# Kernel tuning notes

Hardware: AMD Instinct MI355X
Metric: run time of the kernel (lower is better)

Reference implementation:

```python
import jax, jax.numpy as jnp
import numpy as np

N, E, IN_DIM, OUT_DIM, N_GRAPHS = 50000, 400000, 64, 128, 64


def setup_inputs() -> dict:
    key = jax.random.key(0)
    ks = jax.random.split(key, 16)
    x = jax.random.normal(ks[0], (N, IN_DIM), dtype=jnp.float32)
    edge_index = jax.random.randint(ks[1], (2, E), 0, N, dtype=jnp.int32)
    batch = jnp.sort(jax.random.randint(ks[2], (N,), 0, N_GRAPHS, dtype=jnp.int32))

    def glorot(k, shape):
        lim = np.sqrt(6.0 / (shape[0] + shape[1]))
        return jax.random.uniform(k, shape, jnp.float32, -lim, lim)

    d = IN_DIM
    return {
        "x": x, "edge_index": edge_index, "batch": batch,
        "W1": glorot(ks[3], (d, 2 * d)),     "b1": jnp.zeros((2 * d,), jnp.float32),
        "W2": glorot(ks[4], (2 * d, 4 * d)), "b2": jnp.zeros((4 * d,), jnp.float32),
        "W3": glorot(ks[5], (d, 2 * d)),     "b3": jnp.zeros((2 * d,), jnp.float32),
        "W4": glorot(ks[6], (2 * d, 4 * d)), "b4": jnp.zeros((4 * d,), jnp.float32),
        "W7": glorot(ks[7], (9 * d, OUT_DIM)), "b7": jnp.zeros((OUT_DIM,), jnp.float32),
    }


def _gcn_conv(x, W, b, src, dst, dis):
    # GCNConv: x' = D^{-1/2} (A + I) D^{-1/2} (x W) + b
    h = x @ W                                   # [N, F]
    norm = dis[src] * dis[dst]                  # [E]
    agg = jax.ops.segment_sum(h[src] * norm[:, None], dst, num_segments=N)
    agg = agg + h * (dis * dis)[:, None]        # self-loop contribution
    return agg + b


def reference(x, edge_index, batch, W1, b1, W2, b2, W3, b3, W4, b4, W7, b7):
    src, dst = edge_index[0], edge_index[1]
    # degree of A + I (PyG counts in-degree over columns, +1 for self-loop)
    deg = jax.ops.segment_sum(jnp.ones((E,), x.dtype), dst, num_segments=N) + 1.0
    dis = jax.lax.rsqrt(deg)

    i1 = jnp.tanh(_gcn_conv(x, W1, b1, src, dst, dis))
    i1 = jnp.tanh(_gcn_conv(i1, W2, b2, src, dst, dis))
    i1 = jax.ops.segment_max(i1, batch, num_segments=N_GRAPHS)  # global_max_pool
    i1 = jnp.max(i1, axis=0, keepdims=True)                     # [1, 4d]
    i1 = jnp.broadcast_to(i1, (x.shape[0], i1.shape[1]))        # expand to [N, 4d]

    i2 = jnp.tanh(_gcn_conv(x, W3, b3, src, dst, dis))
    i2 = jnp.tanh(_gcn_conv(i2, W4, b4, src, dst, dis))

    c = jnp.concatenate((i1, i2, x), axis=1)                    # [N, 9d]
    return jnp.tanh(_gcn_conv(c, W7, b7, src, dst, dis))
```

## Files before the change

kernel.cpp:

```cpp
#include <hip/hip_runtime.h>
#include <hip/hip_bf16.h>
#include <cstdint>
#include <cstddef>

#define NN 50000
#define EE 400000

typedef __attribute__((ext_vector_type(8))) __bf16 bf16x8;
typedef __attribute__((ext_vector_type(4))) __bf16 bf16x4;
typedef __attribute__((ext_vector_type(2))) __bf16 bf16x2;
typedef __attribute__((ext_vector_type(4))) float f32x4;

static __device__ __forceinline__ float dec_key(unsigned k) {
  return (k & 0x80000000u) ? __uint_as_float(k & 0x7fffffffu) : __uint_as_float(~k);
}
static __device__ __forceinline__ unsigned enc_key(float f) {
  unsigned b = __float_as_uint(f);
  return (f >= 0.f) ? (b | 0x80000000u) : ~b;
}

__global__ void count_kernel(const int* __restrict__ dst, int* __restrict__ cnt, int e) {
  int i = blockIdx.x * blockDim.x + threadIdx.x;
  if (i < e) atomicAdd(&cnt[dst[i]], 1);
}

__global__ void dis_kernel(const int* __restrict__ cnt, float* __restrict__ dis, int n) {
  int i = blockIdx.x * blockDim.x + threadIdx.x;
  if (i < n) dis[i] = rsqrtf((float)cnt[i] + 1.0f);
}

#define SCAN_CHUNK 1024
__global__ __launch_bounds__(256) void scan1_kernel(const int* __restrict__ cnt,
                                                    int* __restrict__ rowptr,
                                                    int* __restrict__ bsum, int n) {
  int b = blockIdx.x;
  int base = b * SCAN_CHUNK;
  int t = threadIdx.x;
  int v[4];
  int s = 0;
#pragma unroll
  for (int i = 0; i < 4; ++i) {
    int idx = base + t * 4 + i;
    v[i] = (idx < n) ? cnt[idx] : 0;
    s += v[i];
  }
  int lane = t & 63, w = t >> 6;
  int inc = s;
#pragma unroll
  for (int off = 1; off < 64; off <<= 1) {
    int o = __shfl_up(inc, off, 64);
    if (lane >= off) inc += o;
  }
  __shared__ int wsum[4];
  if (lane == 63) wsum[w] = inc;
  __syncthreads();
  int woff = 0;
  for (int i = 0; i < w; ++i) woff += wsum[i];
  int run = woff + inc - s;
#pragma unroll
  for (int i = 0; i < 4; ++i) {
    int idx = base + t * 4 + i;
    if (idx < n) rowptr[idx] = run;
    run += v[i];
  }
  if (t == 255) bsum[b] = woff + inc;
}

__global__ void scan2_kernel(int* __restrict__ bsum, int nb) {
  int t = threadIdx.x;
  int v = (t < nb) ? bsum[t] : 0;
  int s = v;
#pragma unroll
  for (int off = 1; off < 64; off <<= 1) {
    int o = __shfl_up(s, off, 64);
    if (t >= off) s += o;
  }
  if (t < nb) bsum[t] = s - v;
}

__global__ __launch_bounds__(256) void scan3_kernel(int* __restrict__ rowptr,
                                                    const int* __restrict__ bsum, int n, int total) {
  int i = blockIdx.x * blockDim.x + threadIdx.x;
  if (i < n) rowptr[i] += bsum[i >> 10];
  if (i == 0) rowptr[n] = total;
}

__global__ void fill_kernel(const int* __restrict__ src, const int* __restrict__ dst,
                            const int* __restrict__ rowptr, int* __restrict__ cursor,
                            int* __restrict__ col, int e) {
  int i = blockIdx.x * blockDim.x + threadIdx.x;
  if (i < e) {
    int d = dst[i];
    int p = atomicAdd(&cursor[d], 1);
    col[rowptr[d] + p] = src[i];
  }
}

__global__ __launch_bounds__(256) void wcvt_kernel(const float* __restrict__ W,
                                                   __bf16* __restrict__ Wt, int K, int Nout) {
  int idx = blockIdx.x * blockDim.x + threadIdx.x;
  if (idx < K * Nout) {
    int n = idx / K, k = idx - n * K;
    Wt[idx] = (__bf16)W[(size_t)k * Nout + n];
  }
}

__global__ __launch_bounds__(256) void wcat_kernel(const float* __restrict__ W1,
                                                   const float* __restrict__ W3,
                                                   const float* __restrict__ b1,
                                                   const float* __restrict__ b3,
                                                   float* __restrict__ Wcat,
                                                   float* __restrict__ bcat) {
  int idx = blockIdx.x * blockDim.x + threadIdx.x;
  if (idx < 64 * 256) {
    int k = idx >> 8, j = idx & 255;
    Wcat[idx] = (j < 128) ? W1[k * 128 + j] : W3[k * 128 + (j - 128)];
  }
  if (idx < 256) bcat[idx] = (idx < 128) ? b1[idx] : b3[idx - 128];
}

#define BM 64
#define BN 64
#define BK 16

template <typename OT>
__global__ __launch_bounds__(256) void gemm_f32(
    const float* __restrict__ A, const float* __restrict__ W, OT* __restrict__ C,
    int M, int K, int Nout, const float* __restrict__ colAdd, int accumulate, int doTanh) {
  __shared__ float As[BK][BM + 4];
  __shared__ float Ws[BK][BN];
  int tid = threadIdx.x;
  int row0 = blockIdx.x * BM;
  int col0 = blockIdx.y * BN;
  int tx = tid & 15;
  int ty = tid >> 4;
  float acc[4][4] = {};
  for (int k0 = 0; k0 < K; k0 += BK) {
#pragma unroll
    for (int i = 0; i < 4; ++i) {
      int idx = tid + i * 256;
      int r = idx >> 4, c = idx & 15;
      int gr = row0 + r;
      float v = (gr < M) ? A[(size_t)gr * K + k0 + c] : 0.f;
      As[c][r] = v;
    }
#pragma unroll
    for (int i = 0; i < 4; ++i) {
      int idx = tid + i * 256;
      int r = idx >> 6, c = idx & 63;
      Ws[r][c] = W[(size_t)(k0 + r) * Nout + col0 + c];
    }
    __syncthreads();
#pragma unroll
    for (int kk = 0; kk < BK; ++kk) {
      float4 av = *(const float4*)&As[kk][ty * 4];
      float4 wv = *(const float4*)&Ws[kk][tx * 4];
      float a[4] = {av.x, av.y, av.z, av.w};
      float w[4] = {wv.x, wv.y, wv.z, wv.w};
#pragma unroll
      for (int i = 0; i < 4; ++i)
#pragma unroll
        for (int j = 0; j < 4; ++j) acc[i][j] = fmaf(a[i], w[j], acc[i][j]);
    }
    __syncthreads();
  }
#pragma unroll
  for (int i = 0; i < 4; ++i) {
    int gr = row0 + ty * 4 + i;
    if (gr >= M) continue;
#pragma unroll
    for (int j = 0; j < 4; ++j) {
      int gc = col0 + tx * 4 + j;
      size_t idx = (size_t)gr * Nout + gc;
      float v = acc[i][j];
      if (colAdd) v += colAdd[gc];
      if (accumulate) v += (float)C[idx];
      if (doTanh) v = tanhf(v);
      C[idx] = (OT)v;
    }
  }
}

#define TM 128
#define TN 64
#define TK 64

__global__ __launch_bounds__(256) void gemm_mfma(
    const __bf16* __restrict__ A, int lda, const __bf16* __restrict__ Wt,
    float* __restrict__ Cf, __bf16* __restrict__ Ch,
    int M, int K, int Nout, const float* __restrict__ colAdd, int doTanh,
    unsigned* __restrict__ colmaxOut) {
  __shared__ char lds[(TM * TK + TN * TK) * 2];
  char* AsB = lds;
  char* BtB = lds + TM * TK * 2;
  int tid = threadIdx.x;
  int row0 = blockIdx.x * TM;
  int col0 = blockIdx.y * TN;
  int w = tid >> 6, l = tid & 63;
  int lr = l & 15, lh = l >> 4;
  int wmB = (w >> 1) * 64;
  int wnB = (w & 1) * 32;
  f32x4 acc[4][2] = {};
  for (int k0 = 0; k0 < K; k0 += TK) {
    if (k0) __syncthreads();
#pragma unroll
    for (int i = 0; i < 4; ++i) {
      int id = tid + i * 256;
      int r = id >> 3, oc = id & 7;
      int gr = row0 + r;
      bf16x8 sv;
      if (gr < M) sv = *(const bf16x8*)(A + (size_t)gr * lda + k0 + oc * 8);
      else sv = bf16x8{};
      int byte = (r * 128 + oc * 16) ^ ((r & 7) << 4);
      *(bf16x8*)(AsB + byte) = sv;
    }
#pragma unroll
    for (int i = 0; i < 2; ++i) {
      int id = tid + i * 256;
      int c = id >> 3, oc = id & 7;
      bf16x8 sv = *(const bf16x8*)(Wt + (size_t)(col0 + c) * K + k0 + oc * 8);
      int byte = (c * 128 + oc * 16) ^ ((c & 7) << 4);
      *(bf16x8*)(BtB + byte) = sv;
    }
    __syncthreads();
#pragma unroll
    for (int s = 0; s < 2; ++s) {
      bf16x8 af[4], bfr[2];
#pragma unroll
      for (int mi = 0; mi < 4; ++mi) {
        int r = wmB + mi * 16 + lr;
        int byte = (r * 128 + (s * 32 + lh * 8) * 2) ^ ((r & 7) << 4);
        af[mi] = *(const bf16x8*)(AsB + byte);
      }
#pragma unroll
      for (int ni = 0; ni < 2; ++ni) {
        int c = wnB + ni * 16 + lr;
        int byte = (c * 128 + (s * 32 + lh * 8) * 2) ^ ((c & 7) << 4);
        bfr[ni] = *(const bf16x8*)(BtB + byte);
      }
#pragma unroll
      for (int mi = 0; mi < 4; ++mi)
#pragma unroll
        for (int ni = 0; ni < 2; ++ni)
          acc[mi][ni] =
              __builtin_amdgcn_mfma_f32_16x16x32_bf16(af[mi], bfr[ni], acc[mi][ni], 0, 0, 0);
    }
  }
  float cmax[2] = {-3.0e38f, -3.0e38f};
#pragma unroll
  for (int mi = 0; mi < 4; ++mi) {
#pragma unroll
    for (int ni = 0; ni < 2; ++ni) {
#pragma unroll
      for (int r = 0; r < 4; ++r) {
        int gr = row0 + wmB + mi * 16 + lh * 4 + r;
        if (gr >= M) continue;
        int gc = col0 + wnB + ni * 16 + lr;
        size_t idx = (size_t)gr * Nout + gc;
        float v = acc[mi][ni][r];
        if (colAdd) v += colAdd[gc];
        if (doTanh) v = tanhf(v);
        if (colmaxOut) cmax[ni] = fmaxf(cmax[ni], v);
        if (Cf) Cf[idx] = v;
        if (Ch) Ch[idx] = (__bf16)v;
      }
    }
  }
  if (colmaxOut) {
#pragma unroll
    for (int ni = 0; ni < 2; ++ni) {
      float m = cmax[ni];
      m = fmaxf(m, __shfl_xor(m, 16));
      m = fmaxf(m, __shfl_xor(m, 32));
      if (lh == 0) {
        int gc = col0 + wnB + ni * 16 + lr;
        atomicMax(&colmaxOut[gc], enc_key(m));
      }
    }
  }
}

template <int VEC, typename IT>
static __device__ __forceinline__ void loadrow(const IT* p, float (&f)[VEC]) {
  if constexpr (sizeof(IT) == 4) {
    if constexpr (VEC == 4) {
      float4 h = *(const float4*)p;
      f[0] = h.x; f[1] = h.y; f[2] = h.z; f[3] = h.w;
    } else if constexpr (VEC == 2) {
      float2 h = *(const float2*)p;
      f[0] = h.x; f[1] = h.y;
    } else {
      f[0] = p[0];
    }
  } else {
    if constexpr (VEC == 4) {
      bf16x4 h = *(const bf16x4*)p;
      f[0] = (float)h[0]; f[1] = (float)h[1]; f[2] = (float)h[2]; f[3] = (float)h[3];
    } else if constexpr (VEC == 2) {
      bf16x2 h = *(const bf16x2*)p;
      f[0] = (float)h[0]; f[1] = (float)h[1];
    } else {
      f[0] = (float)p[0];
    }
  }
}

template <int F, bool EPI, typename IT, typename OT>
__global__ __launch_bounds__(256) void agg_kernel(
    const IT* __restrict__ H, const int* __restrict__ rowptr, const int* __restrict__ col,
    const float* __restrict__ dis, const float* __restrict__ bias, OT* __restrict__ out, int n) {
  constexpr int VEC = F / 64;
  int wid = (int)((blockIdx.x * blockDim.x + threadIdx.x) >> 6);
  int lane = threadIdx.x & 63;
  if (wid >= n) return;
  int node = __builtin_amdgcn_readfirstlane(wid);
  float dd = dis[node];
  float acc[VEC];
  {
    float h[VEC];
    loadrow<VEC, IT>(H + (size_t)node * F + lane * VEC, h);
#pragma unroll
    for (int i = 0; i < VEC; ++i) acc[i] = h[i] * dd * dd;
  }
  int beg = rowptr[node], end = rowptr[node + 1];
  for (int e = beg; e < end; ++e) {
    int s = col[e];
    float w = dis[s] * dd;
    float h[VEC];
    loadrow<VEC, IT>(H + (size_t)s * F + lane * VEC, h);
#pragma unroll
    for (int i = 0; i < VEC; ++i) acc[i] = fmaf(h[i], w, acc[i]);
  }
  OT* o = out + (size_t)node * F + lane * VEC;
#pragma unroll
  for (int i = 0; i < VEC; ++i) {
    float v = acc[i];
    if constexpr (EPI) v = tanhf(v + bias[lane * VEC + i]);
    o[i] = (OT)v;
  }
}

__global__ __launch_bounds__(128) void crow_kernel(const unsigned* __restrict__ maxkey,
                                                   const float* __restrict__ W7top,
                                                   float* __restrict__ crow) {
  int j = threadIdx.x;
  float s = 0.f;
  for (int f = 0; f < 256; ++f) s = fmaf(tanhf(dec_key(maxkey[f])), W7top[f * 128 + j], s);
  crow[j] = s;
}

extern "C" void kernel_launch(void* const* d_in, const int* in_sizes, int n_in,
                              void* d_out, int out_size, void* d_ws, size_t ws_size,
                              hipStream_t stream) {
  const float* x  = (const float*)d_in[0];
  const int* ei   = (const int*)d_in[1];
  const int* srcp = ei;
  const int* dstp = ei + EE;
  const float* W1 = (const float*)d_in[3];
  const float* b1 = (const float*)d_in[4];
  const float* W2 = (const float*)d_in[5];
  const float* b2 = (const float*)d_in[6];
  const float* W3 = (const float*)d_in[7];
  const float* b3 = (const float*)d_in[8];
  const float* W4 = (const float*)d_in[9];
  const float* b4 = (const float*)d_in[10];
  const float* W7 = (const float*)d_in[11];
  const float* b7 = (const float*)d_in[12];
  float* out = (float*)d_out;

  char* p = (char*)d_ws;
  auto alloc = [&](size_t bytes) -> void* {
    void* r = (void*)p;
    p += (bytes + 255) & ~(size_t)255;
    return r;
  };
  __bf16* T13  = (__bf16*)alloc((size_t)NN * 256 * 2);
  float*  H    = (float*)alloc((size_t)NN * 128 * 4);
  __bf16* Hb13 = (__bf16*)alloc((size_t)NN * 256 * 2);
  __bf16* Bb   = (__bf16*)alloc((size_t)NN * 256 * 2);
  float*  AX   = (float*)alloc((size_t)NN * 64 * 4);
  __bf16* W2t  = (__bf16*)alloc((size_t)256 * 128 * 2);
  __bf16* W4t  = (__bf16*)alloc((size_t)256 * 128 * 2);
  __bf16* W7t  = (__bf16*)alloc((size_t)128 * 256 * 2);
  float*  Wcat = (float*)alloc((size_t)64 * 256 * 4);
  float*  bcat = (float*)alloc(256 * 4);
  float* dis = (float*)alloc((size_t)NN * 4);
  int* cnt = (int*)alloc((size_t)NN * 4);
  int* cursor = (int*)alloc((size_t)NN * 4);
  int* rowptr = (int*)alloc((size_t)(NN + 1) * 4);
  int* col = (int*)alloc((size_t)EE * 4);
  int* bsum = (int*)alloc(64 * 4);
  unsigned* maxkey = (unsigned*)alloc(256 * 4);
  float* crow = (float*)alloc(128 * 4);

  hipMemsetAsync(cnt, 0, (size_t)NN * 4, stream);
  hipMemsetAsync(cursor, 0, (size_t)NN * 4, stream);
  hipMemsetAsync(maxkey, 0, 256 * 4, stream);

  int eb = (EE + 255) / 256;
  int nb = (NN + 255) / 256;
  int nchunks = (NN + SCAN_CHUNK - 1) / SCAN_CHUNK;
  count_kernel<<<eb, 256, 0, stream>>>(dstp, cnt, EE);
  dis_kernel<<<nb, 256, 0, stream>>>(cnt, dis, NN);
  scan1_kernel<<<nchunks, 256, 0, stream>>>(cnt, rowptr, bsum, NN);
  scan2_kernel<<<1, 64, 0, stream>>>(bsum, nchunks);
  scan3_kernel<<<nb, 256, 0, stream>>>(rowptr, bsum, NN, EE);
  fill_kernel<<<eb, 256, 0, stream>>>(srcp, dstp, rowptr, cursor, col, EE);

  wcvt_kernel<<<(256 * 128 + 255) / 256, 256, 0, stream>>>(W2, W2t, 128, 256);
  wcvt_kernel<<<(256 * 128 + 255) / 256, 256, 0, stream>>>(W4, W4t, 128, 256);
  wcvt_kernel<<<(128 * 256 + 255) / 256, 256, 0, stream>>>(W7 + 256 * 128, W7t, 256, 128);
  wcat_kernel<<<(64 * 256 + 255) / 256, 256, 0, stream>>>(W1, W3, b1, b3, Wcat, bcat);

  dim3 gB(256);
  int mrows = (NN + BM - 1) / BM;
  int mrowsT = (NN + TM - 1) / TM;
  int aggB = (NN + 3) / 4;

  agg_kernel<64, false, float, float><<<aggB, gB, 0, stream>>>(x, rowptr, col, dis, nullptr, AX, NN);
  gemm_f32<__bf16><<<dim3(mrows, 4), gB, 0, stream>>>(AX, Wcat, T13, NN, 64, 256, bcat, 0, 1);
  agg_kernel<256, false, __bf16, __bf16><<<aggB, gB, 0, stream>>>(T13, rowptr, col, dis, nullptr, Hb13, NN);
  gemm_mfma<<<dim3(mrowsT, 4), gB, 0, stream>>>(Hb13, 256, W2t, nullptr, nullptr, NN, 128, 256, b2, 0, maxkey);
  gemm_mfma<<<dim3(mrowsT, 4), gB, 0, stream>>>(Hb13 + 128, 256, W4t, nullptr, Bb, NN, 128, 256, b4, 1, nullptr);
  crow_kernel<<<1, 128, 0, stream>>>(maxkey, W7, crow);
  gemm_mfma<<<dim3(mrowsT, 2), gB, 0, stream>>>(Bb, 256, W7t, H, nullptr, NN, 256, 128, crow, 0, nullptr);
  gemm_f32<float><<<dim3(mrows, 2), gB, 0, stream>>>(x, W7 + 512 * 128, H, NN, 64, 128, nullptr, 1, 0);
  agg_kernel<128, true, float, float><<<aggB, gB, 0, stream>>>(H, rowptr, col, dis, b7, out, NN);
}
```

Baseline: 457.4 us.

## Replace atomic column max with per-block partials and halve MFMA row tile

The first MFMA GEMM no longer does a global atomicMax on encoded keys. Each block instead writes its per-wave column maxima to a partial buffer, and a new colreduce kernel reduces those partials, which removes the atomics and the memset. The MFMA row tile also shrinks from 128 to 64 rows, giving twice as many blocks with fewer accumulators each. In exchange this adds a kernel launch and a partial buffer, and weight-tile reuse per block drops.

```diff
diff --git a/kernel.cpp b/kernel.cpp
--- a/kernel.cpp
+++ b/kernel.cpp
@@ -10,14 +10,6 @@
 typedef __attribute__((ext_vector_type(4))) __bf16 bf16x4;
 typedef __attribute__((ext_vector_type(2))) __bf16 bf16x2;
 typedef __attribute__((ext_vector_type(4))) float f32x4;
-
-static __device__ __forceinline__ float dec_key(unsigned k) {
-  return (k & 0x80000000u) ? __uint_as_float(k & 0x7fffffffu) : __uint_as_float(~k);
-}
-static __device__ __forceinline__ unsigned enc_key(float f) {
-  unsigned b = __float_as_uint(f);
-  return (f >= 0.f) ? (b | 0x80000000u) : ~b;
-}
 
 __global__ void count_kernel(const int* __restrict__ dst, int* __restrict__ cnt, int e) {
   int i = blockIdx.x * blockDim.x + threadIdx.x;
@@ -181,15 +173,16 @@
   }
 }
 
-#define TM 128
+#define TM 64
 #define TN 64
 #define TK 64
+#define CSLOTS 1568
 
 __global__ __launch_bounds__(256) void gemm_mfma(
     const __bf16* __restrict__ A, int lda, const __bf16* __restrict__ Wt,
     float* __restrict__ Cf, __bf16* __restrict__ Ch,
     int M, int K, int Nout, const float* __restrict__ colAdd, int doTanh,
-    unsigned* __restrict__ colmaxOut) {
+    float* __restrict__ colmaxPart) {
   __shared__ char lds[(TM * TK + TN * TK) * 2];
   char* AsB = lds;
   char* BtB = lds + TM * TK * 2;
@@ -198,13 +191,13 @@
   int col0 = blockIdx.y * TN;
   int w = tid >> 6, l = tid & 63;
   int lr = l & 15, lh = l >> 4;
-  int wmB = (w >> 1) * 64;
+  int wmB = (w >> 1) * 32;
   int wnB = (w & 1) * 32;
-  f32x4 acc[4][2] = {};
+  f32x4 acc[2][2] = {};
   for (int k0 = 0; k0 < K; k0 += TK) {
     if (k0) __syncthreads();
 #pragma unroll
-    for (int i = 0; i < 4; ++i) {
+    for (int i = 0; i < 2; ++i) {
       int id = tid + i * 256;
       int r = id >> 3, oc = id & 7;
       int gr = row0 + r;
@@ -225,9 +218,9 @@
     __syncthreads();
 #pragma unroll
     for (int s = 0; s < 2; ++s) {
-      bf16x8 af[4], bfr[2];
-#pragma unroll
-      for (int mi = 0; mi < 4; ++mi) {
+      bf16x8 af[2], bfr[2];
+#pragma unroll
+      for (int mi = 0; mi < 2; ++mi) {
         int r = wmB + mi * 16 + lr;
         int byte = (r * 128 + (s * 32 + lh * 8) * 2) ^ ((r & 7) << 4);
         af[mi] = *(const bf16x8*)(AsB + byte);
@@ -239,7 +232,7 @@
         bfr[ni] = *(const bf16x8*)(BtB + byte);
       }
 #pragma unroll
-      for (int mi = 0; mi < 4; ++mi)
+      for (int mi = 0; mi < 2; ++mi)
 #pragma unroll
         for (int ni = 0; ni < 2; ++ni)
           acc[mi][ni] =
@@ -248,7 +241,7 @@
   }
   float cmax[2] = {-3.0e38f, -3.0e38f};
 #pragma unroll
-  for (int mi = 0; mi < 4; ++mi) {
+  for (int mi = 0; mi < 2; ++mi) {
 #pragma unroll
     for (int ni = 0; ni < 2; ++ni) {
 #pragma unroll
@@ -260,13 +253,13 @@
         float v = acc[mi][ni][r];
         if (colAdd) v += colAdd[gc];
         if (doTanh) v = tanhf(v);
-        if (colmaxOut) cmax[ni] = fmaxf(cmax[ni], v);
+        if (colmaxPart) cmax[ni] = fmaxf(cmax[ni], v);
         if (Cf) Cf[idx] = v;
         if (Ch) Ch[idx] = (__bf16)v;
       }
     }
   }
-  if (colmaxOut) {
+  if (colmaxPart) {
 #pragma unroll
     for (int ni = 0; ni < 2; ++ni) {
       float m = cmax[ni];
@@ -274,10 +267,21 @@
       m = fmaxf(m, __shfl_xor(m, 32));
       if (lh == 0) {
         int gc = col0 + wnB + ni * 16 + lr;
-        atomicMax(&colmaxOut[gc], enc_key(m));
+        colmaxPart[(size_t)gc * CSLOTS + blockIdx.x * 2 + (w >> 1)] = m;
       }
     }
   }
+}
+
+__global__ __launch_bounds__(64) void colreduce_kernel(const float* __restrict__ part,
+                                                       float* __restrict__ maxz, int nslots) {
+  int c = blockIdx.x;
+  int t = threadIdx.x;
+  float m = -3.0e38f;
+  for (int i = t; i < nslots; i += 64) m = fmaxf(m, part[(size_t)c * CSLOTS + i]);
+#pragma unroll
+  for (int off = 32; off >= 1; off >>= 1) m = fmaxf(m, __shfl_xor(m, off));
+  if (t == 0) maxz[c] = m;
 }
 
 template <int VEC, typename IT>
@@ -340,12 +344,12 @@
   }
 }
 
-__global__ __launch_bounds__(128) void crow_kernel(const unsigned* __restrict__ maxkey,
+__global__ __launch_bounds__(128) void crow_kernel(const float* __restrict__ maxz,
                                                    const float* __restrict__ W7top,
                                                    float* __restrict__ crow) {
   int j = threadIdx.x;
   float s = 0.f;
-  for (int f = 0; f < 256; ++f) s = fmaf(tanhf(dec_key(maxkey[f])), W7top[f * 128 + j], s);
+  for (int f = 0; f < 256; ++f) s = fmaf(tanhf(maxz[f]), W7top[f * 128 + j], s);
   crow[j] = s;
 }
 
@@ -384,18 +388,18 @@
   __bf16* W7t  = (__bf16*)alloc((size_t)128 * 256 * 2);
   float*  Wcat = (float*)alloc((size_t)64 * 256 * 4);
   float*  bcat = (float*)alloc(256 * 4);
+  float*  cpart = (float*)alloc((size_t)256 * CSLOTS * 4);
+  float*  maxz  = (float*)alloc(256 * 4);
   float* dis = (float*)alloc((size_t)NN * 4);
   int* cnt = (int*)alloc((size_t)NN * 4);
   int* cursor = (int*)alloc((size_t)NN * 4);
   int* rowptr = (int*)alloc((size_t)(NN + 1) * 4);
   int* col = (int*)alloc((size_t)EE * 4);
   int* bsum = (int*)alloc(64 * 4);
-  unsigned* maxkey = (unsigned*)alloc(256 * 4);
   float* crow = (float*)alloc(128 * 4);
 
   hipMemsetAsync(cnt, 0, (size_t)NN * 4, stream);
   hipMemsetAsync(cursor, 0, (size_t)NN * 4, stream);
-  hipMemsetAsync(maxkey, 0, 256 * 4, stream);
 
   int eb = (EE + 255) / 256;
   int nb = (NN + 255) / 256;
@@ -420,9 +424,10 @@
   agg_kernel<64, false, float, float><<<aggB, gB, 0, stream>>>(x, rowptr, col, dis, nullptr, AX, NN);
   gemm_f32<__bf16><<<dim3(mrows, 4), gB, 0, stream>>>(AX, Wcat, T13, NN, 64, 256, bcat, 0, 1);
   agg_kernel<256, false, __bf16, __bf16><<<aggB, gB, 0, stream>>>(T13, rowptr, col, dis, nullptr, Hb13, NN);
-  gemm_mfma<<<dim3(mrowsT, 4), gB, 0, stream>>>(Hb13, 256, W2t, nullptr, nullptr, NN, 128, 256, b2, 0, maxkey);
+  gemm_mfma<<<dim3(mrowsT, 4), gB, 0, stream>>>(Hb13, 256, W2t, nullptr, nullptr, NN, 128, 256, b2, 0, cpart);
+  colreduce_kernel<<<256, 64, 0, stream>>>(cpart, maxz, mrowsT * 2);
   gemm_mfma<<<dim3(mrowsT, 4), gB, 0, stream>>>(Hb13 + 128, 256, W4t, nullptr, Bb, NN, 128, 256, b4, 1, nullptr);
-  crow_kernel<<<1, 128, 0, stream>>>(maxkey, W7, crow);
+  crow_kernel<<<1, 128, 0, stream>>>(maxz, W7, crow);
   gemm_mfma<<<dim3(mrowsT, 2), gB, 0, stream>>>(Bb, 256, W7t, H, nullptr, NN, 256, 128, crow, 0, nullptr);
   gemm_f32<float><<<dim3(mrows, 2), gB, 0, stream>>>(x, W7 + 512 * 128, H, NN, 64, 128, nullptr, 1, 0);
   agg_kernel<128, true, float, float><<<aggB, gB, 0, stream>>>(H, rowptr, col, dis, b7, out, NN);
```

After: 424.2 us. 7.3% less time.
